# Performance work log

Measured on AMD Instinct MI355X. Metric: run time of the kernel, lower is better.

## Reference

```python
import jax, jax.numpy as jnp
import numpy as np

EPS = 1e-5

def _bn(x, g, b, m, v):
    # inference-mode batchnorm with moving statistics
    return (x - m) * jax.lax.rsqrt(v + EPS) * g + b

def setup_inputs() -> dict:
    key = jax.random.key(0)
    ks = jax.random.split(key, 12)
    t, b, s, hu = 512, 64, 1024, 1024
    d_in = s + hu
    si = jax.random.normal(ks[0], (b, s), dtype=jnp.float32)
    h = jax.random.normal(ks[1], (t, b, hu), dtype=jnp.float32)
    W0 = jax.random.normal(ks[2], (d_in, 10), dtype=jnp.float32) * 0.02
    b0 = jnp.zeros((10,), jnp.float32)
    g0 = jnp.ones((10,), jnp.float32)
    be0 = jnp.zeros((10,), jnp.float32)
    m0 = jax.random.normal(ks[3], (10,), dtype=jnp.float32) * 0.1
    v0 = jax.random.uniform(ks[4], (10,), dtype=jnp.float32) + 0.5
    W1 = jax.random.normal(ks[5], (10, 5), dtype=jnp.float32) * 0.3
    b1 = jnp.zeros((5,), jnp.float32)
    g1 = jnp.ones((5,), jnp.float32)
    be1 = jnp.zeros((5,), jnp.float32)
    m1 = jax.random.normal(ks[6], (5,), dtype=jnp.float32) * 0.1
    v1 = jax.random.uniform(ks[7], (5,), dtype=jnp.float32) + 0.5
    W2 = jax.random.normal(ks[8], (5, 1), dtype=jnp.float32) * 0.4
    b2 = jnp.zeros((1,), jnp.float32)
    return {"si": si, "h": h, "W0": W0, "b0": b0, "g0": g0, "be0": be0,
            "m0": m0, "v0": v0, "W1": W1, "b1": b1, "g1": g1, "be1": be1,
            "m1": m1, "v1": v1, "W2": W2, "b2": b2}

def reference(si, h, W0, b0, g0, be0, m0, v0, W1, b1, g1, be1, m1, v1, W2, b2):
    t, b, hu = h.shape
    # concat decoder state with every encoder hidden state: [t, b, s+hu]
    x = jnp.concatenate([jnp.broadcast_to(si[None], (t,) + si.shape), h], axis=-1)
    x = jax.nn.relu(_bn(x @ W0 + b0, g0, be0, m0, v0))
    x = jax.nn.relu(_bn(x @ W1 + b1, g1, be1, m1, v1))
    scores = x @ W2 + b2                       # [t, b, 1]
    # original: tf.concat over axis 0 -> [t*b, 1], softmax over axis 0 (ALL t*b entries)
    a = jax.nn.softmax(scores.reshape(t * b))  # [t*b]
    # original uses only the first t rows of the flattened softmax as scalar weights
    ci = jnp.einsum('t,tbh->bh', a[:t], h)     # [b, hu]
    return ci
```

## Files before the change

### kernel.cpp

```cpp
#include <hip/hip_runtime.h>

#define EPS 1e-5f

constexpr int T  = 512;
constexpr int B  = 64;
constexpr int HU = 1024;
constexpr int S  = 1024;
constexpr int P  = T * B;
constexpr int C  = B * HU;
constexpr int TSPLIT = 16;

constexpr size_t OFF_SIW0   = 0;
constexpr size_t OFF_SCORES = 1024;
constexpr size_t OFF_A      = 34816;
constexpr size_t OFF_PART   = 35840;

__global__ __launch_bounds__(256) void k_siw0(const float* __restrict__ si,
                                              const float* __restrict__ W0,
                                              float* __restrict__ out) {
    const int b   = blockIdx.x;
    const int tid = threadIdx.x;
    const float4 sv = ((const float4*)(si + (size_t)b * S))[tid];
    const float* wp = W0 + (size_t)(4 * tid) * 10;

    float acc[10];
#pragma unroll
    for (int j = 0; j < 10; ++j) acc[j] = 0.f;
#pragma unroll
    for (int d = 0; d < 4; ++d) {
        const float hx = (&sv.x)[d];
#pragma unroll
        for (int j = 0; j < 10; ++j) acc[j] = fmaf(hx, wp[d * 10 + j], acc[j]);
    }
#pragma unroll
    for (int j = 0; j < 10; ++j) {
#pragma unroll
        for (int off = 32; off > 0; off >>= 1)
            acc[j] += __shfl_down(acc[j], off, 64);
    }
    __shared__ float red[4][10];
    const int wv = tid >> 6, ln = tid & 63;
    if (ln == 0) {
#pragma unroll
        for (int j = 0; j < 10; ++j) red[wv][j] = acc[j];
    }
    __syncthreads();
    if (tid < 10)
        out[(size_t)b * 10 + tid] =
            red[0][tid] + red[1][tid] + red[2][tid] + red[3][tid];
}

__global__ __launch_bounds__(256) void k_scores(
    const float* __restrict__ h,  const float* __restrict__ W0,
    const float* __restrict__ siW0,
    const float* __restrict__ b0, const float* __restrict__ g0,
    const float* __restrict__ be0,const float* __restrict__ m0,
    const float* __restrict__ v0,
    const float* __restrict__ W1, const float* __restrict__ b1,
    const float* __restrict__ g1, const float* __restrict__ be1,
    const float* __restrict__ m1, const float* __restrict__ v1,
    const float* __restrict__ W2, const float* __restrict__ b2,
    float* __restrict__ scores) {
    const int t   = blockIdx.x;
    const int tid = threadIdx.x;
    const int wv  = tid >> 6;
    const int ln  = tid & 63;
    const float* hblk = h + (size_t)t * 64 * HU;

    __shared__ float lds[64 * 256];
    __shared__ float s_part[4][64][10];

    float acc[10];
#pragma unroll
    for (int j = 0; j < 10; ++j) acc[j] = 0.f;

    for (int cc = 0; cc < 4; ++cc) {
        if (cc) __syncthreads();
        const float* hc = hblk + cc * 256;
#pragma unroll
        for (int it = 0; it < 16; ++it) {
            const int f = it * 256 + tid;
            const int r = f >> 6;
            const int q = f & 63;
            const float4 v = *(const float4*)(hc + (size_t)r * HU + q * 4);
            *(float4*)(&lds[r * 256 + ((q ^ r) << 2)]) = v;
        }
        __syncthreads();
        const int qbase = __builtin_amdgcn_readfirstlane(wv * 16);
#pragma unroll
        for (int qi = 0; qi < 16; ++qi) {
            const int qq = qbase + qi;
            const float4 hv =
                *(const float4*)(&lds[ln * 256 + ((qq ^ ln) << 2)]);
            const float* wp = W0 + (size_t)(1024 + cc * 256 + qq * 4) * 10;
#pragma unroll
            for (int d = 0; d < 4; ++d) {
                const float hx = (&hv.x)[d];
#pragma unroll
                for (int j = 0; j < 10; ++j)
                    acc[j] = fmaf(hx, wp[d * 10 + j], acc[j]);
            }
        }
    }

#pragma unroll
    for (int j = 0; j < 10; ++j) s_part[wv][ln][j] = acc[j];
    __syncthreads();

    if (wv == 0) {
        float y[10];
#pragma unroll
        for (int j = 0; j < 10; ++j) {
            float u = s_part[0][ln][j] + s_part[1][ln][j] + s_part[2][ln][j] +
                      s_part[3][ln][j] + siW0[(size_t)ln * 10 + j] + b0[j];
            u = (u - m0[j]) * (1.0f / sqrtf(v0[j] + EPS)) * g0[j] + be0[j];
            y[j] = fmaxf(u, 0.f);
        }
        float z[5];
#pragma unroll
        for (int i = 0; i < 5; ++i) {
            float u = b1[i];
#pragma unroll
            for (int j = 0; j < 10; ++j) u = fmaf(y[j], W1[j * 5 + i], u);
            u = (u - m1[i]) * (1.0f / sqrtf(v1[i] + EPS)) * g1[i] + be1[i];
            z[i] = fmaxf(u, 0.f);
        }
        float sc = b2[0];
#pragma unroll
        for (int i = 0; i < 5; ++i) sc = fmaf(z[i], W2[i], sc);
        scores[t * 64 + ln] = sc;
    }
}

__global__ __launch_bounds__(1024) void k_softmax(const float* __restrict__ scores,
                                                  float* __restrict__ a) {
    const int tid = threadIdx.x;
    __shared__ float red[16];
    __shared__ float s_m, s_z;

    float v[32];
#pragma unroll
    for (int i = 0; i < 32; ++i) v[i] = scores[tid + i * 1024];

    float mx = v[0];
#pragma unroll
    for (int i = 1; i < 32; ++i) mx = fmaxf(mx, v[i]);
#pragma unroll
    for (int off = 32; off > 0; off >>= 1)
        mx = fmaxf(mx, __shfl_down(mx, off, 64));
    if ((tid & 63) == 0) red[tid >> 6] = mx;
    __syncthreads();
    if (tid == 0) {
        float m = red[0];
        for (int i = 1; i < 16; ++i) m = fmaxf(m, red[i]);
        s_m = m;
    }
    __syncthreads();
    const float m = s_m;

    float sum = 0.f;
#pragma unroll
    for (int i = 0; i < 32; ++i) sum += __expf(v[i] - m);
#pragma unroll
    for (int off = 32; off > 0; off >>= 1)
        sum += __shfl_down(sum, off, 64);
    if ((tid & 63) == 0) red[tid >> 6] = sum;
    __syncthreads();
    if (tid == 0) {
        float z = 0.f;
        for (int i = 0; i < 16; ++i) z += red[i];
        s_z = z;
    }
    __syncthreads();

    if (tid < T) a[tid] = expf(scores[tid] - m) / s_z;
}

__global__ __launch_bounds__(256) void k_wsum(const float* __restrict__ h,
                                              const float* __restrict__ a,
                                              float* __restrict__ part) {
    const int cb = blockIdx.x & 63;
    const int ts = blockIdx.x >> 6;
    const int c  = cb * 1024 + threadIdx.x * 4;
    const float* hp = h + (size_t)ts * 32 * C + c;
    const float* ap = a + ts * 32;

    float4 acc = {0.f, 0.f, 0.f, 0.f};
#pragma unroll 4
    for (int i = 0; i < 32; ++i) {
        const float av = ap[i];
        const float4 hv = *(const float4*)(hp + (size_t)i * C);
        acc.x = fmaf(av, hv.x, acc.x);
        acc.y = fmaf(av, hv.y, acc.y);
        acc.z = fmaf(av, hv.z, acc.z);
        acc.w = fmaf(av, hv.w, acc.w);
    }
    *(float4*)(part + (size_t)ts * C + c) = acc;
}

__global__ __launch_bounds__(256) void k_reduce(const float* __restrict__ part,
                                                float* __restrict__ out) {
    const int c = blockIdx.x * 1024 + threadIdx.x * 4;
    float4 s = {0.f, 0.f, 0.f, 0.f};
#pragma unroll
    for (int ts = 0; ts < TSPLIT; ++ts) {
        const float4 v = *(const float4*)(part + (size_t)ts * C + c);
        s.x += v.x; s.y += v.y; s.z += v.z; s.w += v.w;
    }
    *(float4*)(out + c) = s;
}

extern "C" void kernel_launch(void* const* d_in, const int* in_sizes, int n_in,
                              void* d_out, int out_size, void* d_ws, size_t ws_size,
                              hipStream_t stream) {
    const float* si  = (const float*)d_in[0];
    const float* h   = (const float*)d_in[1];
    const float* W0  = (const float*)d_in[2];
    const float* b0  = (const float*)d_in[3];
    const float* g0  = (const float*)d_in[4];
    const float* be0 = (const float*)d_in[5];
    const float* m0  = (const float*)d_in[6];
    const float* v0  = (const float*)d_in[7];
    const float* W1  = (const float*)d_in[8];
    const float* b1  = (const float*)d_in[9];
    const float* g1  = (const float*)d_in[10];
    const float* be1 = (const float*)d_in[11];
    const float* m1  = (const float*)d_in[12];
    const float* v1  = (const float*)d_in[13];
    const float* W2  = (const float*)d_in[14];
    const float* b2  = (const float*)d_in[15];

    float* ws     = (float*)d_ws;
    float* siW0   = ws + OFF_SIW0;
    float* scores = ws + OFF_SCORES;
    float* a      = ws + OFF_A;
    float* part   = ws + OFF_PART;
    float* out    = (float*)d_out;

    hipLaunchKernelGGL(k_siw0,    dim3(64),   dim3(256),  0, stream, si, W0, siW0);
    hipLaunchKernelGGL(k_scores,  dim3(512),  dim3(256),  0, stream, h, W0, siW0,
                       b0, g0, be0, m0, v0, W1, b1, g1, be1, m1, v1, W2, b2, scores);
    hipLaunchKernelGGL(k_softmax, dim3(1),    dim3(1024), 0, stream, scores, a);
    hipLaunchKernelGGL(k_wsum,    dim3(1024), dim3(256),  0, stream, h, a, part);
    hipLaunchKernelGGL(k_reduce,  dim3(64),   dim3(256),  0, stream, part, out);
}
```

Before: 274.9 us.

## Prefetch next h chunk into registers and fold reduction into atomic adds

k_scores now loads the next 256-column chunk of h into registers while the current chunk is consumed from LDS. Each block starts at a rotated chunk so that blocks do not all touch the same W0 rows at once, and a launch bound asking for two blocks per CU is added. The separate k_reduce kernel and its partial buffer are removed: k_wsum atomically adds its partial sums into the output, which k_siw0 now zeroes first. This hides global-load latency and saves a launch plus the partial write and read, at the cost of higher register pressure and non-deterministic float summation order.

Result: slower. 308.4 us (+12.2%).

```diff
diff --git a/kernel.cpp b/kernel.cpp
--- a/kernel.cpp
+++ b/kernel.cpp
@@ -13,13 +13,17 @@
 constexpr size_t OFF_SIW0   = 0;
 constexpr size_t OFF_SCORES = 1024;
 constexpr size_t OFF_A      = 34816;
-constexpr size_t OFF_PART   = 35840;
 
 __global__ __launch_bounds__(256) void k_siw0(const float* __restrict__ si,
                                               const float* __restrict__ W0,
+                                              float* __restrict__ siW0,
                                               float* __restrict__ out) {
     const int b   = blockIdx.x;
     const int tid = threadIdx.x;
+
+    const float4 z4 = {0.f, 0.f, 0.f, 0.f};
+    *(float4*)(out + (size_t)b * 1024 + tid * 4) = z4;
+
     const float4 sv = ((const float4*)(si + (size_t)b * S))[tid];
     const float* wp = W0 + (size_t)(4 * tid) * 10;
 
@@ -46,11 +50,11 @@
     }
     __syncthreads();
     if (tid < 10)
-        out[(size_t)b * 10 + tid] =
+        siW0[(size_t)b * 10 + tid] =
             red[0][tid] + red[1][tid] + red[2][tid] + red[3][tid];
 }
 
-__global__ __launch_bounds__(256) void k_scores(
+__global__ __launch_bounds__(256, 2) void k_scores(
     const float* __restrict__ h,  const float* __restrict__ W0,
     const float* __restrict__ siW0,
     const float* __restrict__ b0, const float* __restrict__ g0,
@@ -70,29 +74,44 @@
     __shared__ float lds[64 * 256];
     __shared__ float s_part[4][64][10];
 
+    const int r_base = tid >> 6;
+    const int q      = tid & 63;
+
+    float4 buf[16];
+    const int c_first = t & 3;
+#pragma unroll
+    for (int it = 0; it < 16; ++it) {
+        const int r = it * 4 + r_base;
+        buf[it] = *(const float4*)(hblk + (size_t)r * HU + c_first * 256 + q * 4);
+    }
+
     float acc[10];
 #pragma unroll
     for (int j = 0; j < 10; ++j) acc[j] = 0.f;
 
-    for (int cc = 0; cc < 4; ++cc) {
-        if (cc) __syncthreads();
-        const float* hc = hblk + cc * 256;
+    for (int i = 0; i < 4; ++i) {
+        const int c = (c_first + i) & 3;
+        if (i) __syncthreads();
 #pragma unroll
         for (int it = 0; it < 16; ++it) {
-            const int f = it * 256 + tid;
-            const int r = f >> 6;
-            const int q = f & 63;
-            const float4 v = *(const float4*)(hc + (size_t)r * HU + q * 4);
-            *(float4*)(&lds[r * 256 + ((q ^ r) << 2)]) = v;
+            const int r = it * 4 + r_base;
+            *(float4*)(&lds[r * 256 + ((q ^ r) << 2)]) = buf[it];
         }
         __syncthreads();
+        if (i < 3) {
+            const int cn = (c_first + i + 1) & 3;
+#pragma unroll
+            for (int it = 0; it < 16; ++it) {
+                const int r = it * 4 + r_base;
+                buf[it] = *(const float4*)(hblk + (size_t)r * HU + cn * 256 + q * 4);
+            }
+        }
         const int qbase = __builtin_amdgcn_readfirstlane(wv * 16);
 #pragma unroll
         for (int qi = 0; qi < 16; ++qi) {
             const int qq = qbase + qi;
-            const float4 hv =
-                *(const float4*)(&lds[ln * 256 + ((qq ^ ln) << 2)]);
-            const float* wp = W0 + (size_t)(1024 + cc * 256 + qq * 4) * 10;
+            const float4 hv = *(const float4*)(&lds[ln * 256 + ((qq ^ ln) << 2)]);
+            const float* wp = W0 + (size_t)(1024 + c * 256 + qq * 4) * 10;
 #pragma unroll
             for (int d = 0; d < 4; ++d) {
                 const float hx = (&hv.x)[d];
@@ -178,7 +197,7 @@
 
 __global__ __launch_bounds__(256) void k_wsum(const float* __restrict__ h,
                                               const float* __restrict__ a,
-                                              float* __restrict__ part) {
+                                              float* __restrict__ out) {
     const int cb = blockIdx.x & 63;
     const int ts = blockIdx.x >> 6;
     const int c  = cb * 1024 + threadIdx.x * 4;
@@ -195,19 +214,10 @@
         acc.z = fmaf(av, hv.z, acc.z);
         acc.w = fmaf(av, hv.w, acc.w);
     }
-    *(float4*)(part + (size_t)ts * C + c) = acc;
-}
-
-__global__ __launch_bounds__(256) void k_reduce(const float* __restrict__ part,
-                                                float* __restrict__ out) {
-    const int c = blockIdx.x * 1024 + threadIdx.x * 4;
-    float4 s = {0.f, 0.f, 0.f, 0.f};
-#pragma unroll
-    for (int ts = 0; ts < TSPLIT; ++ts) {
-        const float4 v = *(const float4*)(part + (size_t)ts * C + c);
-        s.x += v.x; s.y += v.y; s.z += v.z; s.w += v.w;
-    }
-    *(float4*)(out + c) = s;
+    atomicAdd(out + c + 0, acc.x);
+    atomicAdd(out + c + 1, acc.y);
+    atomicAdd(out + c + 2, acc.z);
+    atomicAdd(out + c + 3, acc.w);
 }
 
 extern "C" void kernel_launch(void* const* d_in, const int* in_sizes, int n_in,
@@ -234,13 +244,11 @@
     float* siW0   = ws + OFF_SIW0;
     float* scores = ws + OFF_SCORES;
     float* a      = ws + OFF_A;
-    float* part   = ws + OFF_PART;
     float* out    = (float*)d_out;
 
-    hipLaunchKernelGGL(k_siw0,    dim3(64),   dim3(256),  0, stream, si, W0, siW0);
+    hipLaunchKernelGGL(k_siw0,    dim3(64),   dim3(256),  0, stream, si, W0, siW0, out);
     hipLaunchKernelGGL(k_scores,  dim3(512),  dim3(256),  0, stream, h, W0, siW0,
                        b0, g0, be0, m0, v0, W1, b1, g1, be1, m1, v1, W2, b2, scores);
     hipLaunchKernelGGL(k_softmax, dim3(1),    dim3(1024), 0, stream, scores, a);
-    hipLaunchKernelGGL(k_wsum,    dim3(1024), dim3(256),  0, stream, h, a, part);
-    hipLaunchKernelGGL(k_reduce,  dim3(64),   dim3(256),  0, stream, part, out);
-}
+    hipLaunchKernelGGL(k_wsum,    dim3(1024), dim3(256),  0, stream, h, a, out);
+}
```
